# Optimization experiments

Measured on AMD Instinct MI355X. Metric: run time of the kernel, lower is better.

## Reference

```python
import jax, jax.numpy as jnp
import numpy as np

B, S, DM, H, DF = 2, 2048, 1024, 16, 4096
HD = DM // H
EPS = 1e-6
NEG = -1e9


def setup_inputs() -> dict:
    key = jax.random.key(0)
    ks = jax.random.split(key, 16)
    sc = 1.0 / np.sqrt(DM)
    scf = 1.0 / np.sqrt(DF)
    return {
        "x": jax.random.normal(ks[0], (B, S, DM), jnp.float32),
        "src_mask": jax.random.randint(ks[1], (B, 1, 1, S), 0, 2, jnp.int32),
        "Wq": jax.random.normal(ks[2], (DM, DM), jnp.float32) * sc,
        "bq": jnp.zeros((DM,), jnp.float32),
        "Wk": jax.random.normal(ks[3], (DM, DM), jnp.float32) * sc,
        "bk": jnp.zeros((DM,), jnp.float32),
        "Wv": jax.random.normal(ks[4], (DM, DM), jnp.float32) * sc,
        "bv": jnp.zeros((DM,), jnp.float32),
        "Wo": jax.random.normal(ks[5], (DM, DM), jnp.float32) * sc,
        "bo": jnp.zeros((DM,), jnp.float32),
        "W1": jax.random.normal(ks[6], (DM, DF), jnp.float32) * sc,
        "b1": jnp.zeros((DF,), jnp.float32),
        "W2": jax.random.normal(ks[7], (DF, DM), jnp.float32) * scf,
        "b2": jnp.zeros((DM,), jnp.float32),
        "alpha1": jnp.ones((1,), jnp.float32),
        "beta1": jnp.ones((1,), jnp.float32),
        "alpha2": jnp.ones((1,), jnp.float32),
        "beta2": jnp.ones((1,), jnp.float32),
    }


def layer_norm(x, alpha, beta):
    # torch: mean + unbiased std (ddof=1), scalar alpha/beta, eps added to std
    mean = jnp.mean(x, axis=-1, keepdims=True)
    std = jnp.std(x, axis=-1, keepdims=True, ddof=1)
    return alpha * (x - mean) / (std + EPS) + beta


def mha(x, mask, Wq, bq, Wk, bk, Wv, bv, Wo, bo):
    def split(t):  # [B,S,DM] -> [B,H,S,HD]
        return t.reshape(B, S, H, HD).transpose(0, 2, 1, 3)
    q = split(x @ Wq + bq)
    k = split(x @ Wk + bk)
    v = split(x @ Wv + bv)
    scores = jnp.einsum("bhqd,bhkd->bhqk", q, k) / np.sqrt(HD)
    scores = jnp.where(mask == 0, NEG, scores)
    probs = jax.nn.softmax(scores, axis=-1)  # dropout in eval mode = identity
    out = jnp.einsum("bhqk,bhkd->bhqd", probs, v)
    out = out.transpose(0, 2, 1, 3).reshape(B, S, DM)
    return out @ Wo + bo


def reference(x, src_mask, Wq, bq, Wk, bk, Wv, bv, Wo, bo, W1, b1, W2, b2,
              alpha1, beta1, alpha2, beta2):
    # pre-norm residual: x + attn(norm(x)); dropout disabled (eval)
    n1 = layer_norm(x, alpha1, beta1)
    h = x + mha(n1, src_mask, Wq, bq, Wk, bk, Wv, bv, Wo, bo)
    n2 = layer_norm(h, alpha2, beta2)
    ff = jax.nn.relu(n2 @ W1 + b1) @ W2 + b2
    return h + ff
```

## Files before the change

### kernel.cpp

```cpp
#include <hip/hip_runtime.h>
#include <hip/hip_bf16.h>

#define SEQ   2048
#define BATCH 2
#define DMODEL 1024
#define DFF   4096
#define NHEAD 16
#define HDIM  64
#define NTOK  (BATCH*SEQ)

typedef short s8v __attribute__((ext_vector_type(8)));
typedef float f4v __attribute__((ext_vector_type(4)));

__device__ __forceinline__ float b2f(unsigned short u) {
    union { unsigned int i; float f; } v; v.i = ((unsigned int)u) << 16; return v.f;
}
__device__ __forceinline__ unsigned short f2b(float f) {
    union { unsigned int i; float f; } v; v.f = f;
    unsigned int r = v.i + 0x7FFFu + ((v.i >> 16) & 1u);
    return (unsigned short)(r >> 16);
}
__device__ __forceinline__ ushort2 cvt_pk(float a, float b) {
    __hip_bfloat162 h = __float22bfloat162_rn(float2{ a, b });
    return *(ushort2*)&h;
}

__device__ __forceinline__ f4v mfma_bf16(s8v a, s8v b, f4v c) {
    return __builtin_amdgcn_mfma_f32_16x16x32_bf16(a, b, c, 0, 0, 0);
}

__device__ __forceinline__ void gload_lds16(const void* g, void* l) {
    __builtin_amdgcn_global_load_lds(
        (const __attribute__((address_space(1))) unsigned int*)g,
        (__attribute__((address_space(3))) unsigned int*)l, 16, 0, 0);
}

template<int N> __device__ __forceinline__ void wait_vmcnt() {
    if constexpr (N == 8)      asm volatile("s_waitcnt vmcnt(8)" ::: "memory");
    else if constexpr (N == 6) asm volatile("s_waitcnt vmcnt(6)" ::: "memory");
    else                       asm volatile("s_waitcnt vmcnt(0)" ::: "memory");
}

__device__ __forceinline__ void tp_tile(const float* __restrict__ src,
                                        unsigned short* __restrict__ dst,
                                        int R, int C, int br, int bc, int t,
                                        unsigned short* tl) {
    for (int i = 0; i < 16; i++) {
        int idx = t + 256 * i;
        int r = idx >> 6, c = idx & 63;
        tl[r * 65 + c] = f2b(src[(size_t)(br * 64 + r) * C + bc * 64 + c]);
    }
    __syncthreads();
    for (int i = 0; i < 16; i++) {
        int idx = t + 256 * i;
        int r2 = idx >> 6, c2 = idx & 63;
        dst[(size_t)(bc * 64 + r2) * R + br * 64 + c2] = tl[c2 * 65 + r2];
    }
}

__global__ __launch_bounds__(256) void prep_weights(const float* __restrict__ Wq,
                                                    const float* __restrict__ Wk,
                                                    const float* __restrict__ Wv,
                                                    const float* __restrict__ Wo,
                                                    const float* __restrict__ W1,
                                                    const float* __restrict__ W2,
                                                    const float* __restrict__ bq,
                                                    const float* __restrict__ bk,
                                                    const float* __restrict__ bv,
                                                    const int* __restrict__ msk,
                                                    const float* __restrict__ x,
                                                    const float* __restrict__ a1,
                                                    const float* __restrict__ be1,
                                                    unsigned short* __restrict__ Wqkv_t,
                                                    unsigned short* __restrict__ Wo_t,
                                                    unsigned short* __restrict__ W1_t,
                                                    unsigned short* __restrict__ W2_t,
                                                    float* __restrict__ bqkv,
                                                    float* __restrict__ maskf,
                                                    unsigned short* __restrict__ n1) {
    __shared__ unsigned short tl[64 * 65];
    __shared__ float red[8];
    const int t = threadIdx.x;
    const int bx = blockIdx.x, by = blockIdx.y, z = blockIdx.z;
    if (z < 4) {
        const float* src = (z == 0) ? Wq : (z == 1) ? Wk : (z == 2) ? Wv : Wo;
        unsigned short* dst = (z == 3) ? Wo_t : Wqkv_t + (size_t)z * 1024 * 1024;
        tp_tile(src, dst, 1024, 1024, bx, by, t, tl);
    } else if (z == 4) {
        for (int i = 0; i < 4; i++) {
            tp_tile(W1, W1_t, 1024, 4096, bx, by + 16 * i, t, tl);
            __syncthreads();
        }
    } else if (z == 5) {
        if (bx == 0 && by == 0) {
            for (int i = 0; i < 12; i++) {
                int idx = t + 256 * i;
                if (idx < 1024) bqkv[idx] = bq[idx];
                else if (idx < 2048) bqkv[idx] = bk[idx - 1024];
                else if (idx < 3072) bqkv[idx] = bv[idx - 2048];
            }
        }
        if (bx == 1 && by == 0) {
            for (int i = 0; i < 16; i++) {
                int idx = t + 256 * i;
                maskf[idx] = (msk[idx] == 0) ? -1e9f : 0.f;
            }
        }
        for (int i = 0; i < 4; i++) {
            tp_tile(W2, W2_t, 4096, 1024, bx + 16 * i, by, t, tl);
            __syncthreads();
        }
    } else {
        const int row = (z - 6) * 256 + by * 16 + bx;
        const float* xr = x + (size_t)row * DMODEL;
        float4 u = ((const float4*)xr)[t];
        float v[4] = { u.x, u.y, u.z, u.w };
        float s = v[0] + v[1] + v[2] + v[3];
        float sq = v[0]*v[0] + v[1]*v[1] + v[2]*v[2] + v[3]*v[3];
        for (int off = 32; off; off >>= 1) { s += __shfl_xor(s, off); sq += __shfl_xor(sq, off); }
        int wave = t >> 6, lane = t & 63;
        if (!lane) { red[wave] = s; red[4 + wave] = sq; }
        __syncthreads();
        s = red[0] + red[1] + red[2] + red[3];
        sq = red[4] + red[5] + red[6] + red[7];
        float mean = s * (1.f / DMODEL);
        float var = (sq - (float)DMODEL * mean * mean) * (1.f / (DMODEL - 1));
        var = var < 0.f ? 0.f : var;
        float inv = a1[0] / (sqrtf(var) + 1e-6f);
        float bt = be1[0];
        uint2 ou;
        unsigned short r0 = f2b((v[0] - mean) * inv + bt);
        unsigned short r1 = f2b((v[1] - mean) * inv + bt);
        unsigned short r2 = f2b((v[2] - mean) * inv + bt);
        unsigned short r3 = f2b((v[3] - mean) * inv + bt);
        ou.x = (unsigned int)r0 | ((unsigned int)r1 << 16);
        ou.y = (unsigned int)r2 | ((unsigned int)r3 << 16);
        ((uint2*)(n1 + (size_t)row * DMODEL))[t] = ou;
    }
}

__global__ __launch_bounds__(256) void pack_kv(const unsigned short* __restrict__ Kb,
                                               const unsigned short* __restrict__ Vb,
                                               unsigned short* __restrict__ Kc,
                                               unsigned short* __restrict__ Vc) {
    __shared__ unsigned short tl[64 * 65];
    const int t = threadIdx.x;
    const int kt = blockIdx.x, h = blockIdx.y, b = blockIdx.z;
    const unsigned short* srcK = Kb + (size_t)b * SEQ * 1024 + h * HDIM;
    unsigned short* dstK = Kc + ((size_t)((b * NHEAD + h) * 32 + kt)) * 4096;
    for (int i = 0; i < 2; i++) {
        int ci = t + 256 * i;
        int r = ci >> 3, cp = ci & 7;
        int cl = cp ^ (r & 7);
        *(uint4*)&dstK[ci * 8] = *(const uint4*)&srcK[(size_t)(kt * 64 + r) * 1024 + cl * 8];
    }
    const unsigned short* srcV = Vb + (size_t)b * SEQ * 1024 + h * HDIM;
    for (int i = 0; i < 16; i++) {
        int idx = t + 256 * i;
        int r = idx >> 6, c = idx & 63;
        tl[r * 65 + c] = srcV[(size_t)(kt * 64 + r) * 1024 + c];
    }
    __syncthreads();
    unsigned short* dstV = Vc + ((size_t)((b * NHEAD + h) * 32 + kt)) * 4096;
    for (int i = 0; i < 2; i++) {
        int ci = t + 256 * i;
        int r = ci >> 3, cp = ci & 7;
        int cl = cp ^ (r & 7);
        ushort4 e0, e1;
        e0.x = tl[(cl * 8 + 0) * 65 + r]; e0.y = tl[(cl * 8 + 1) * 65 + r];
        e0.z = tl[(cl * 8 + 2) * 65 + r]; e0.w = tl[(cl * 8 + 3) * 65 + r];
        e1.x = tl[(cl * 8 + 4) * 65 + r]; e1.y = tl[(cl * 8 + 5) * 65 + r];
        e1.z = tl[(cl * 8 + 6) * 65 + r]; e1.w = tl[(cl * 8 + 7) * 65 + r];
        *(ushort4*)&dstV[ci * 8]     = e0;
        *(ushort4*)&dstV[ci * 8 + 4] = e1;
    }
}

__global__ __launch_bounds__(256) void ln_kernel(const float* __restrict__ x,
                                                 const float* __restrict__ al,
                                                 const float* __restrict__ be,
                                                 unsigned short* __restrict__ o) {
    const int row = blockIdx.x;
    const float* xr = x + (size_t)row * DMODEL;
    float4 u = ((const float4*)xr)[threadIdx.x];
    float v[4] = { u.x, u.y, u.z, u.w };
    float s = v[0] + v[1] + v[2] + v[3];
    float sq = v[0]*v[0] + v[1]*v[1] + v[2]*v[2] + v[3]*v[3];
    for (int off = 32; off; off >>= 1) { s += __shfl_xor(s, off); sq += __shfl_xor(sq, off); }
    __shared__ float red[8];
    int wave = threadIdx.x >> 6, lane = threadIdx.x & 63;
    if (!lane) { red[wave] = s; red[4 + wave] = sq; }
    __syncthreads();
    s = red[0] + red[1] + red[2] + red[3];
    sq = red[4] + red[5] + red[6] + red[7];
    float mean = s * (1.f / DMODEL);
    float var = (sq - (float)DMODEL * mean * mean) * (1.f / (DMODEL - 1));
    var = var < 0.f ? 0.f : var;
    float inv = al[0] / (sqrtf(var) + 1e-6f);
    float bt = be[0];
    uint2 ou;
    unsigned short r0 = f2b((v[0] - mean) * inv + bt);
    unsigned short r1 = f2b((v[1] - mean) * inv + bt);
    unsigned short r2 = f2b((v[2] - mean) * inv + bt);
    unsigned short r3 = f2b((v[3] - mean) * inv + bt);
    ou.x = (unsigned int)r0 | ((unsigned int)r1 << 16);
    ou.y = (unsigned int)r2 | ((unsigned int)r3 << 16);
    ((uint2*)(o + (size_t)row * DMODEL))[threadIdx.x] = ou;
}

template<bool RELU, bool RES, typename CT, bool SPLIT3 = false>
__global__ __launch_bounds__(256) void gemm_bt(const unsigned short* __restrict__ A,
                                               const unsigned short* __restrict__ Bt,
                                               const float* __restrict__ bias,
                                               const float* __restrict__ res,
                                               CT* __restrict__ C,
                                               int M, int N, int K) {
    __shared__ __align__(16) unsigned short smA[128 * 32];
    __shared__ __align__(16) unsigned short smB[128 * 32];
    const int t = threadIdx.x;
    const int wave = t >> 6, lane = t & 63;
    const int quad = lane >> 4, l16 = lane & 15;
    const int wm = wave & 1, wn = wave >> 1;
    const int m0 = blockIdx.x * 128, n0 = blockIdx.y * 128;

    f4v acc[4][4] = {};

    const int c0 = t, c1 = t + 256;
    const int rA0 = c0 >> 2, sA0 = c0 & 3;
    const int rA1 = c1 >> 2, sA1 = c1 & 3;

    for (int k0 = 0; k0 < K; k0 += 32) {
        __syncthreads();
        gload_lds16(A  + (size_t)(m0 + rA0) * K + k0 + sA0 * 8, smA + c0 * 8);
        gload_lds16(A  + (size_t)(m0 + rA1) * K + k0 + sA1 * 8, smA + c1 * 8);
        gload_lds16(Bt + (size_t)(n0 + rA0) * K + k0 + sA0 * 8, smB + c0 * 8);
        gload_lds16(Bt + (size_t)(n0 + rA1) * K + k0 + sA1 * 8, smB + c1 * 8);
        __syncthreads();
        s8v a[4], b[4];
        for (int i = 0; i < 4; i++)
            a[i] = *(const s8v*)&smA[(wm * 64 + i * 16 + l16) * 32 + quad * 8];
        for (int i = 0; i < 4; i++)
            b[i] = *(const s8v*)&smB[(wn * 64 + i * 16 + l16) * 32 + quad * 8];
        for (int mi = 0; mi < 4; mi++)
            for (int ni = 0; ni < 4; ni++)
                acc[mi][ni] = mfma_bf16(a[mi], b[ni], acc[mi][ni]);
    }

    for (int mi = 0; mi < 4; mi++) {
        for (int ni = 0; ni < 4; ni++) {
            int col = n0 + wn * 64 + ni * 16 + l16;
            float bv = bias[col];
            for (int r = 0; r < 4; r++) {
                int row = m0 + wm * 64 + mi * 16 + quad * 4 + r;
                float v = acc[mi][ni][r] + bv;
                if (RELU) v = v > 0.f ? v : 0.f;
                if (RES) v += res[(size_t)row * N + col];
                size_t cidx;
                if constexpr (SPLIT3)
                    cidx = (size_t)(col >> 10) * ((size_t)NTOK * 1024)
                         + (size_t)row * 1024 + (col & 1023);
                else
                    cidx = (size_t)row * N + col;
                if constexpr (sizeof(CT) == 2)
                    C[cidx] = f2b(v);
                else
                    C[cidx] = v;
            }
        }
    }
}


template<int BROWS>
__device__ __forceinline__ void stage256(const unsigned short* __restrict__ A,
                                         const unsigned short* __restrict__ Bt,
                                         int m0, int n0, int K, int k0,
                                         unsigned short* sA, unsigned short* sB, int t) {
#pragma unroll
    for (int i = 0; i < 4; i++) {
        int ci = i * 512 + t;
        int r = ci >> 3, c = (ci & 7) ^ (r & 7);
        gload_lds16(A + (size_t)(m0 + r) * K + k0 + c * 8, sA + (size_t)ci * 8);
    }
#pragma unroll
    for (int i = 0; i < BROWS / 64; i++) {
        int ci = i * 512 + t;
        int r = ci >> 3, c = (ci & 7) ^ (r & 7);
        gload_lds16(Bt + (size_t)(n0 + r) * K + k0 + c * 8, sB + (size_t)ci * 8);
    }
}

template<int NFC>
__device__ __forceinline__ void comp256(const unsigned short* sA, const unsigned short* sB,
                                        int wm, int wn, int l16, int quad,
                                        f4v acc[8][NFC]) {
#pragma unroll
    for (int s = 0; s < 2; s++) {
        s8v b[NFC];
#pragma unroll
        for (int ni = 0; ni < NFC; ni++) {
            int r = wn * (NFC * 16) + ni * 16 + l16;
            int p = (s * 4 + quad) ^ (r & 7);
            b[ni] = *(const s8v*)&sB[r * 64 + p * 8];
        }
#pragma unroll
        for (int mi = 0; mi < 8; mi++) {
            int r = wm * 128 + mi * 16 + l16;
            int p = (s * 4 + quad) ^ (r & 7);
            s8v a = *(const s8v*)&sA[r * 64 + p * 8];
#pragma unroll
            for (int ni = 0; ni < NFC; ni++)
                acc[mi][ni] = mfma_bf16(a, b[ni], acc[mi][ni]);
        }
    }
}

template<bool RELU, bool RES, typename CT, bool SPLIT3, int BN>
__global__ __launch_bounds__(512, 2) void gemm256(const unsigned short* __restrict__ A,
                                                  const unsigned short* __restrict__ Bt,
                                                  const float* __restrict__ bias,
                                                  const float* __restrict__ res,
                                                  CT* __restrict__ C,
                                                  float* __restrict__ pbuf,
                                                  int M, int N, int K, int KS) {
    constexpr int NFC = BN / 64;
    constexpr int LPT = 4 + BN / 64;
    __shared__ __align__(16) unsigned short smA[2][256 * 64];
    __shared__ __align__(16) unsigned short smB[2][BN * 64];
    const int t = threadIdx.x;
    const int wave = t >> 6, lane = t & 63;
    const int quad = lane >> 4, l16 = lane & 15;
    const int wm = wave >> 2, wn = wave & 3;
    const int m0 = blockIdx.x * 256, n0 = blockIdx.y * BN;
    const int z = blockIdx.z;
    const int kbeg = z * KS;
    const int nt = KS >> 6;

    f4v acc[8][NFC] = {};

    stage256<BN>(A, Bt, m0, n0, K, kbeg,      smA[0], smB[0], t);
    stage256<BN>(A, Bt, m0, n0, K, kbeg + 64, smA[1], smB[1], t);
    wait_vmcnt<LPT>();
    __builtin_amdgcn_s_barrier();

    for (int it = 0; it < nt - 2; ++it) {
        const int cb = it & 1;
        __builtin_amdgcn_s_setprio(1);
        comp256<NFC>(smA[cb], smB[cb], wm, wn, l16, quad, acc);
        __builtin_amdgcn_s_setprio(0);
        asm volatile("s_waitcnt lgkmcnt(0)" ::: "memory");
        __builtin_amdgcn_s_barrier();
        stage256<BN>(A, Bt, m0, n0, K, kbeg + (it + 2) * 64, smA[cb], smB[cb], t);
        wait_vmcnt<LPT>();
        __builtin_amdgcn_s_barrier();
    }
    {
        const int cb = (nt - 2) & 1;
        __builtin_amdgcn_s_setprio(1);
        comp256<NFC>(smA[cb], smB[cb], wm, wn, l16, quad, acc);
        __builtin_amdgcn_s_setprio(0);
        asm volatile("s_waitcnt vmcnt(0)" ::: "memory");
        __builtin_amdgcn_s_barrier();
    }
    {
        const int cb = (nt - 1) & 1;
        __builtin_amdgcn_s_setprio(1);
        comp256<NFC>(smA[cb], smB[cb], wm, wn, l16, quad, acc);
        __builtin_amdgcn_s_setprio(0);
    }

#pragma unroll
    for (int mi = 0; mi < 8; mi++) {
#pragma unroll
        for (int ni = 0; ni < NFC; ni++) {
            const int col = n0 + wn * (NFC * 16) + ni * 16 + l16;
            const int row0 = m0 + wm * 128 + mi * 16 + quad * 4;
            if (z == 0) {
                const float bv = bias[col];
#pragma unroll
                for (int r = 0; r < 4; r++) {
                    float v = acc[mi][ni][r] + bv;
                    if (RELU) v = v > 0.f ? v : 0.f;
                    if (RES) v += res[(size_t)(row0 + r) * N + col];
                    size_t cidx;
                    if constexpr (SPLIT3)
                        cidx = (size_t)(col >> 10) * ((size_t)NTOK * 1024)
                             + (size_t)(row0 + r) * 1024 + (col & 1023);
                    else
                        cidx = (size_t)(row0 + r) * N + col;
                    if constexpr (sizeof(CT) == 2)
                        C[cidx] = f2b(v);
                    else
                        C[cidx] = v;
                }
            } else {
#pragma unroll
                for (int r = 0; r < 4; r++)
                    pbuf[(size_t)(z - 1) * M * N + (size_t)(row0 + r) * N + col]
                        = acc[mi][ni][r];
            }
        }
    }
}

__global__ __launch_bounds__(256) void add_pbuf(float* __restrict__ out,
                                                const float* __restrict__ pbuf) {
    const int i0 = (blockIdx.x * 256 + threadIdx.x) * 8;
    float4 a0 = *(const float4*)&out[i0];
    float4 a1 = *(const float4*)&out[i0 + 4];
    float4 p0 = *(const float4*)&pbuf[i0];
    float4 p1 = *(const float4*)&pbuf[i0 + 4];
    a0.x += p0.x; a0.y += p0.y; a0.z += p0.z; a0.w += p0.w;
    a1.x += p1.x; a1.y += p1.y; a1.z += p1.z; a1.w += p1.w;
    *(float4*)&out[i0]     = a0;
    *(float4*)&out[i0 + 4] = a1;
}

__global__ __launch_bounds__(256) void attn_kernel(const unsigned short* __restrict__ Qb,
                                                   const unsigned short* __restrict__ Kc,
                                                   const unsigned short* __restrict__ Vc,
                                                   const float* __restrict__ maskf,
                                                   unsigned short* __restrict__ out) {
    __shared__ __align__(16) unsigned short smK[4096];
    __shared__ __align__(16) unsigned short smV[4096];
    __shared__ __align__(16) unsigned short smP[4][16 * 72];

    const int t = threadIdx.x;
    const int wave = t >> 6, lane = t & 63;
    const int quad = lane >> 4, l16 = lane & 15;
    const int qt = blockIdx.x, h = blockIdx.y, b = blockIdx.z;
    const int q0 = qt * 64 + wave * 16;
    const unsigned short* Kbh = Kc + ((size_t)(b * NHEAD + h)) * 32 * 4096;
    const unsigned short* Vbh = Vc + ((size_t)(b * NHEAD + h)) * 32 * 4096;
    const float* mrow = maskf + b * SEQ;
    unsigned short* smPw = &smP[wave][0];

    const unsigned short* Qp = Qb + ((size_t)b * SEQ + q0 + l16) * 1024 + h * HDIM + quad * 8;
    s8v qf0 = *(const s8v*)(Qp);
    s8v qf1 = *(const s8v*)(Qp + 32);

    float l_s = 0.f;
    f4v oacc[4] = {};

    for (int kt = 0; kt < 32; kt++) {
        const int k0 = kt * 64;
        const unsigned short* ks = Kbh + kt * 4096;
        const unsigned short* vs = Vbh + kt * 4096;
        __syncthreads();
        gload_lds16(ks + t * 8,           smK + t * 8);
        gload_lds16(ks + (t + 256) * 8,   smK + (t + 256) * 8);
        gload_lds16(vs + t * 8,           smV + t * 8);
        gload_lds16(vs + (t + 256) * 8,   smV + (t + 256) * 8);
        __syncthreads();

        f4v s[4];
        for (int kt4 = 0; kt4 < 4; kt4++) {
            int r = kt4 * 16 + l16, sw = r & 7;
            s8v kf0 = *(const s8v*)&smK[r * 64 + ((quad ^ sw) * 8)];
            s8v kf1 = *(const s8v*)&smK[r * 64 + (((quad + 4) ^ sw) * 8)];
            f4v z = {};
            z = mfma_bf16(kf0, qf0, z);
            z = mfma_bf16(kf1, qf1, z);
            s[kt4] = z;
        }
        for (int kt4 = 0; kt4 < 4; kt4++) {
            float4 mf = *(const float4*)&mrow[k0 + kt4 * 16 + quad * 4];
            s[kt4][0] = s[kt4][0] * 0.125f + mf.x;
            s[kt4][1] = s[kt4][1] * 0.125f + mf.y;
            s[kt4][2] = s[kt4][2] * 0.125f + mf.z;
            s[kt4][3] = s[kt4][3] * 0.125f + mf.w;
        }
        for (int kt4 = 0; kt4 < 4; kt4++)
            for (int r = 0; r < 4; r++) {
                float p = __expf(s[kt4][r]);
                s[kt4][r] = p;
                l_s += p;
            }
        for (int kt4 = 0; kt4 < 4; kt4++) {
            ushort2 p01 = cvt_pk(s[kt4][0], s[kt4][1]);
            ushort2 p23 = cvt_pk(s[kt4][2], s[kt4][3]);
            ushort4 pk;
            pk.x = p01.x; pk.y = p01.y; pk.z = p23.x; pk.w = p23.y;
            *(ushort4*)&smPw[l16 * 72 + kt4 * 16 + quad * 4] = pk;
        }
        s8v pf0 = *(const s8v*)&smPw[l16 * 72 + quad * 8];
        s8v pf1 = *(const s8v*)&smPw[l16 * 72 + quad * 8 + 32];
        for (int nt = 0; nt < 4; nt++) {
            int r = nt * 16 + l16, sw = r & 7;
            s8v v0 = *(const s8v*)&smV[r * 64 + ((quad ^ sw) * 8)];
            s8v v1 = *(const s8v*)&smV[r * 64 + (((quad + 4) ^ sw) * 8)];
            oacc[nt] = mfma_bf16(pf0, v0, oacc[nt]);
            oacc[nt] = mfma_bf16(pf1, v1, oacc[nt]);
        }
    }

    l_s += __shfl_xor(l_s, 16);
    l_s += __shfl_xor(l_s, 32);
    float lrr[4];
    for (int r = 0; r < 4; r++) lrr[r] = __shfl(l_s, quad * 4 + r);
    for (int nt = 0; nt < 4; nt++)
        for (int r = 0; r < 4; r++) {
            int row = q0 + quad * 4 + r;
            int col = h * HDIM + nt * 16 + l16;
            out[((size_t)b * SEQ + row) * DMODEL + col] = f2b(oacc[nt][r] / lrr[r]);
        }
}

extern "C" void kernel_launch(void* const* d_in, const int* in_sizes, int n_in,
                              void* d_out, int out_size, void* d_ws, size_t ws_size,
                              hipStream_t stream) {
    const float* x   = (const float*)d_in[0];
    const int*   msk = (const int*)d_in[1];
    const float* Wq  = (const float*)d_in[2];
    const float* bq  = (const float*)d_in[3];
    const float* Wk  = (const float*)d_in[4];
    const float* bk  = (const float*)d_in[5];
    const float* Wv  = (const float*)d_in[6];
    const float* bv  = (const float*)d_in[7];
    const float* Wo  = (const float*)d_in[8];
    const float* bo  = (const float*)d_in[9];
    const float* W1  = (const float*)d_in[10];
    const float* b1  = (const float*)d_in[11];
    const float* W2  = (const float*)d_in[12];
    const float* b2  = (const float*)d_in[13];
    const float* a1  = (const float*)d_in[14];
    const float* be1 = (const float*)d_in[15];
    const float* a2  = (const float*)d_in[16];
    const float* be2 = (const float*)d_in[17];
    float* outf = (float*)d_out;

    char* ws = (char*)d_ws;
    const size_t MB = 1024 * 1024;
    unsigned short* W2_t   = (unsigned short*)(ws);
    unsigned short* W1_t   = (unsigned short*)(ws + 8 * MB);
    float*          Pbuf   = (float*)(ws + 8 * MB);
    unsigned short* Wqkv_t = (unsigned short*)(ws + 16 * MB);
    float*          bqkv   = (float*)(ws + 22 * MB);
    unsigned short* Kc     = (unsigned short*)(ws + 16 * MB);
    unsigned short* n2     = (unsigned short*)(ws + 16 * MB);
    unsigned short* Wo_t   = (unsigned short*)(ws + 24 * MB);
    unsigned short* Qb     = (unsigned short*)(ws + 26 * MB);
    unsigned short* Kb     = (unsigned short*)(ws + 34 * MB);
    unsigned short* Vb     = (unsigned short*)(ws + 42 * MB);
    unsigned short* ff1    = (unsigned short*)(ws + 26 * MB);
    unsigned short* attnO  = (unsigned short*)(ws + 50 * MB);
    unsigned short* n1     = (unsigned short*)d_out;
    float*          maskf  = (float*)((char*)d_out + 8 * MB);
    unsigned short* Vc     = (unsigned short*)d_out;
    float*          hbuf   = (float*)d_out;

    prep_weights<<<dim3(16, 16, 22), 256, 0, stream>>>(
        Wq, Wk, Wv, Wo, W1, W2, bq, bk, bv, msk, x, a1, be1,
        Wqkv_t, Wo_t, W1_t, W2_t, bqkv, maskf, n1);

    gemm256<false, false, unsigned short, true, 256><<<dim3(16, 12, 1), 512, 0, stream>>>(
        n1, Wqkv_t, bqkv, nullptr, Qb, nullptr, NTOK, 3072, 1024, 1024);
    pack_kv<<<dim3(32, 16, 2), 256, 0, stream>>>(Kb, Vb, Kc, Vc);
    attn_kernel<<<dim3(32, 16, 2), 256, 0, stream>>>(Qb, Kc, Vc, maskf, attnO);
    gemm_bt<false, true, float><<<dim3(32, 8), 256, 0, stream>>>(
        attnO, Wo_t, bo, x, hbuf, NTOK, 1024, 1024);
    ln_kernel<<<NTOK, 256, 0, stream>>>(hbuf, a2, be2, n2);
    gemm256<true, false, unsigned short, false, 256><<<dim3(16, 16, 1), 512, 0, stream>>>(
        n2, W1_t, b1, nullptr, ff1, nullptr, NTOK, DFF, 1024, 1024);
    gemm256<false, true, float, false, 128><<<dim3(16, 8, 2), 512, 0, stream>>>(
        ff1, W2_t, b2, hbuf, outf, Pbuf, NTOK, 1024, 4096, 2048);
    add_pbuf<<<dim3(2048), 256, 0, stream>>>(outf, Pbuf);
}
```

Baseline: 381.0 us.

## Double-buffer attention K/V tiles and move Wo projection to split-K gemm256

The attention kernel now runs 512 threads per block (128 queries) and double-buffers K/V tiles in LDS. It prefetches the next tile with async global-to-LDS loads while the current one is computed, stages the mask in LDS, and uses a swizzled P buffer with raised wave priority. The output projection drops the old 128x128 gemm_bt for the larger-tile gemm256 path with split-K over two partial buffers plus an add_pbuf pass. The intent is to hide load latency and reuse K/V across more queries, at the cost of an extra launch and more LDS per block.

```diff
diff --git a/kernel.cpp b/kernel.cpp
--- a/kernel.cpp
+++ b/kernel.cpp
@@ -38,6 +38,7 @@
 template<int N> __device__ __forceinline__ void wait_vmcnt() {
     if constexpr (N == 8)      asm volatile("s_waitcnt vmcnt(8)" ::: "memory");
     else if constexpr (N == 6) asm volatile("s_waitcnt vmcnt(6)" ::: "memory");
+    else if constexpr (N == 2) asm volatile("s_waitcnt vmcnt(2)" ::: "memory");
     else                       asm volatile("s_waitcnt vmcnt(0)" ::: "memory");
 }
 
@@ -208,69 +209,6 @@
     ((uint2*)(o + (size_t)row * DMODEL))[threadIdx.x] = ou;
 }
 
-template<bool RELU, bool RES, typename CT, bool SPLIT3 = false>
-__global__ __launch_bounds__(256) void gemm_bt(const unsigned short* __restrict__ A,
-                                               const unsigned short* __restrict__ Bt,
-                                               const float* __restrict__ bias,
-                                               const float* __restrict__ res,
-                                               CT* __restrict__ C,
-                                               int M, int N, int K) {
-    __shared__ __align__(16) unsigned short smA[128 * 32];
-    __shared__ __align__(16) unsigned short smB[128 * 32];
-    const int t = threadIdx.x;
-    const int wave = t >> 6, lane = t & 63;
-    const int quad = lane >> 4, l16 = lane & 15;
-    const int wm = wave & 1, wn = wave >> 1;
-    const int m0 = blockIdx.x * 128, n0 = blockIdx.y * 128;
-
-    f4v acc[4][4] = {};
-
-    const int c0 = t, c1 = t + 256;
-    const int rA0 = c0 >> 2, sA0 = c0 & 3;
-    const int rA1 = c1 >> 2, sA1 = c1 & 3;
-
-    for (int k0 = 0; k0 < K; k0 += 32) {
-        __syncthreads();
-        gload_lds16(A  + (size_t)(m0 + rA0) * K + k0 + sA0 * 8, smA + c0 * 8);
-        gload_lds16(A  + (size_t)(m0 + rA1) * K + k0 + sA1 * 8, smA + c1 * 8);
-        gload_lds16(Bt + (size_t)(n0 + rA0) * K + k0 + sA0 * 8, smB + c0 * 8);
-        gload_lds16(Bt + (size_t)(n0 + rA1) * K + k0 + sA1 * 8, smB + c1 * 8);
-        __syncthreads();
-        s8v a[4], b[4];
-        for (int i = 0; i < 4; i++)
-            a[i] = *(const s8v*)&smA[(wm * 64 + i * 16 + l16) * 32 + quad * 8];
-        for (int i = 0; i < 4; i++)
-            b[i] = *(const s8v*)&smB[(wn * 64 + i * 16 + l16) * 32 + quad * 8];
-        for (int mi = 0; mi < 4; mi++)
-            for (int ni = 0; ni < 4; ni++)
-                acc[mi][ni] = mfma_bf16(a[mi], b[ni], acc[mi][ni]);
-    }
-
-    for (int mi = 0; mi < 4; mi++) {
-        for (int ni = 0; ni < 4; ni++) {
-            int col = n0 + wn * 64 + ni * 16 + l16;
-            float bv = bias[col];
-            for (int r = 0; r < 4; r++) {
-                int row = m0 + wm * 64 + mi * 16 + quad * 4 + r;
-                float v = acc[mi][ni][r] + bv;
-                if (RELU) v = v > 0.f ? v : 0.f;
-                if (RES) v += res[(size_t)row * N + col];
-                size_t cidx;
-                if constexpr (SPLIT3)
-                    cidx = (size_t)(col >> 10) * ((size_t)NTOK * 1024)
-                         + (size_t)row * 1024 + (col & 1023);
-                else
-                    cidx = (size_t)row * N + col;
-                if constexpr (sizeof(CT) == 2)
-                    C[cidx] = f2b(v);
-                else
-                    C[cidx] = v;
-            }
-        }
-    }
-}
-
-
 template<int BROWS>
 __device__ __forceinline__ void stage256(const unsigned short* __restrict__ A,
                                          const unsigned short* __restrict__ Bt,
@@ -416,82 +354,118 @@
     *(float4*)&out[i0 + 4] = a1;
 }
 
-__global__ __launch_bounds__(256) void attn_kernel(const unsigned short* __restrict__ Qb,
+__device__ __forceinline__ void attn_tile(const unsigned short* __restrict__ smKb,
+                                          const unsigned short* __restrict__ smVb,
+                                          const float* __restrict__ smM, int k0,
+                                          unsigned short* __restrict__ smPw,
+                                          s8v qf0, s8v qf1, int quad, int l16,
+                                          float& l_s, f4v* oacc) {
+    const int l7 = l16 & 7;
+    f4v s[4];
+#pragma unroll
+    for (int kt4 = 0; kt4 < 4; kt4++) {
+        int r = kt4 * 16 + l16;
+        s8v kf0 = *(const s8v*)&smKb[r * 64 + ((quad ^ l7) * 8)];
+        s8v kf1 = *(const s8v*)&smKb[r * 64 + (((quad + 4) ^ l7) * 8)];
+        f4v z = {};
+        z = mfma_bf16(kf0, qf0, z);
+        z = mfma_bf16(kf1, qf1, z);
+        s[kt4] = z;
+    }
+#pragma unroll
+    for (int kt4 = 0; kt4 < 4; kt4++) {
+        float4 mf = *(const float4*)&smM[k0 + kt4 * 16 + quad * 4];
+        s[kt4][0] = s[kt4][0] * 0.125f + mf.x;
+        s[kt4][1] = s[kt4][1] * 0.125f + mf.y;
+        s[kt4][2] = s[kt4][2] * 0.125f + mf.z;
+        s[kt4][3] = s[kt4][3] * 0.125f + mf.w;
+    }
+#pragma unroll
+    for (int kt4 = 0; kt4 < 4; kt4++)
+#pragma unroll
+        for (int r = 0; r < 4; r++) {
+            float p = __expf(s[kt4][r]);
+            s[kt4][r] = p;
+            l_s += p;
+        }
+#pragma unroll
+    for (int kt4 = 0; kt4 < 4; kt4++) {
+        ushort2 p01 = cvt_pk(s[kt4][0], s[kt4][1]);
+        ushort2 p23 = cvt_pk(s[kt4][2], s[kt4][3]);
+        ushort4 pk;
+        pk.x = p01.x; pk.y = p01.y; pk.z = p23.x; pk.w = p23.y;
+        int c = kt4 * 2 + (quad >> 1);
+        *(ushort4*)&smPw[l16 * 64 + ((c ^ l7) * 8 + (quad & 1) * 4)] = pk;
+    }
+    s8v pf0 = *(const s8v*)&smPw[l16 * 64 + ((quad ^ l7) * 8)];
+    s8v pf1 = *(const s8v*)&smPw[l16 * 64 + (((quad + 4) ^ l7) * 8)];
+#pragma unroll
+    for (int nt = 0; nt < 4; nt++) {
+        int r = nt * 16 + l16;
+        s8v v0 = *(const s8v*)&smVb[r * 64 + ((quad ^ l7) * 8)];
+        s8v v1 = *(const s8v*)&smVb[r * 64 + (((quad + 4) ^ l7) * 8)];
+        oacc[nt] = mfma_bf16(pf0, v0, oacc[nt]);
+        oacc[nt] = mfma_bf16(pf1, v1, oacc[nt]);
+    }
+}
+
+__global__ __launch_bounds__(512) void attn_kernel(const unsigned short* __restrict__ Qb,
                                                    const unsigned short* __restrict__ Kc,
                                                    const unsigned short* __restrict__ Vc,
                                                    const float* __restrict__ maskf,
                                                    unsigned short* __restrict__ out) {
-    __shared__ __align__(16) unsigned short smK[4096];
-    __shared__ __align__(16) unsigned short smV[4096];
-    __shared__ __align__(16) unsigned short smP[4][16 * 72];
+    __shared__ __align__(16) unsigned short smK[2][4096];
+    __shared__ __align__(16) unsigned short smV[2][4096];
+    __shared__ __align__(16) unsigned short smP[8][1024];
+    __shared__ __align__(16) float smM[SEQ];
 
     const int t = threadIdx.x;
     const int wave = t >> 6, lane = t & 63;
     const int quad = lane >> 4, l16 = lane & 15;
     const int qt = blockIdx.x, h = blockIdx.y, b = blockIdx.z;
-    const int q0 = qt * 64 + wave * 16;
+    const int q0 = qt * 128 + wave * 16;
     const unsigned short* Kbh = Kc + ((size_t)(b * NHEAD + h)) * 32 * 4096;
     const unsigned short* Vbh = Vc + ((size_t)(b * NHEAD + h)) * 32 * 4096;
-    const float* mrow = maskf + b * SEQ;
     unsigned short* smPw = &smP[wave][0];
 
     const unsigned short* Qp = Qb + ((size_t)b * SEQ + q0 + l16) * 1024 + h * HDIM + quad * 8;
     s8v qf0 = *(const s8v*)(Qp);
     s8v qf1 = *(const s8v*)(Qp + 32);
 
+    gload_lds16(maskf + (size_t)b * SEQ + t * 4, (float*)smM + t * 4);
+    gload_lds16(Kbh + t * 8,        smK[0] + t * 8);
+    gload_lds16(Vbh + t * 8,        smV[0] + t * 8);
+    gload_lds16(Kbh + 4096 + t * 8, smK[1] + t * 8);
+    gload_lds16(Vbh + 4096 + t * 8, smV[1] + t * 8);
+    wait_vmcnt<2>();
+    __builtin_amdgcn_s_barrier();
+
     float l_s = 0.f;
     f4v oacc[4] = {};
 
-    for (int kt = 0; kt < 32; kt++) {
-        const int k0 = kt * 64;
-        const unsigned short* ks = Kbh + kt * 4096;
-        const unsigned short* vs = Vbh + kt * 4096;
-        __syncthreads();
-        gload_lds16(ks + t * 8,           smK + t * 8);
-        gload_lds16(ks + (t + 256) * 8,   smK + (t + 256) * 8);
-        gload_lds16(vs + t * 8,           smV + t * 8);
-        gload_lds16(vs + (t + 256) * 8,   smV + (t + 256) * 8);
-        __syncthreads();
-
-        f4v s[4];
-        for (int kt4 = 0; kt4 < 4; kt4++) {
-            int r = kt4 * 16 + l16, sw = r & 7;
-            s8v kf0 = *(const s8v*)&smK[r * 64 + ((quad ^ sw) * 8)];
-            s8v kf1 = *(const s8v*)&smK[r * 64 + (((quad + 4) ^ sw) * 8)];
-            f4v z = {};
-            z = mfma_bf16(kf0, qf0, z);
-            z = mfma_bf16(kf1, qf1, z);
-            s[kt4] = z;
-        }
-        for (int kt4 = 0; kt4 < 4; kt4++) {
-            float4 mf = *(const float4*)&mrow[k0 + kt4 * 16 + quad * 4];
-            s[kt4][0] = s[kt4][0] * 0.125f + mf.x;
-            s[kt4][1] = s[kt4][1] * 0.125f + mf.y;
-            s[kt4][2] = s[kt4][2] * 0.125f + mf.z;
-            s[kt4][3] = s[kt4][3] * 0.125f + mf.w;
-        }
-        for (int kt4 = 0; kt4 < 4; kt4++)
-            for (int r = 0; r < 4; r++) {
-                float p = __expf(s[kt4][r]);
-                s[kt4][r] = p;
-                l_s += p;
-            }
-        for (int kt4 = 0; kt4 < 4; kt4++) {
-            ushort2 p01 = cvt_pk(s[kt4][0], s[kt4][1]);
-            ushort2 p23 = cvt_pk(s[kt4][2], s[kt4][3]);
-            ushort4 pk;
-            pk.x = p01.x; pk.y = p01.y; pk.z = p23.x; pk.w = p23.y;
-            *(ushort4*)&smPw[l16 * 72 + kt4 * 16 + quad * 4] = pk;
-        }
-        s8v pf0 = *(const s8v*)&smPw[l16 * 72 + quad * 8];
-        s8v pf1 = *(const s8v*)&smPw[l16 * 72 + quad * 8 + 32];
-        for (int nt = 0; nt < 4; nt++) {
-            int r = nt * 16 + l16, sw = r & 7;
-            s8v v0 = *(const s8v*)&smV[r * 64 + ((quad ^ sw) * 8)];
-            s8v v1 = *(const s8v*)&smV[r * 64 + (((quad + 4) ^ sw) * 8)];
-            oacc[nt] = mfma_bf16(pf0, v0, oacc[nt]);
-            oacc[nt] = mfma_bf16(pf1, v1, oacc[nt]);
-        }
+    for (int it = 0; it < 30; ++it) {
+        const int cb = it & 1;
+        __builtin_amdgcn_s_setprio(1);
+        attn_tile(smK[cb], smV[cb], smM, it * 64, smPw, qf0, qf1, quad, l16, l_s, oacc);
+        __builtin_amdgcn_s_setprio(0);
+        asm volatile("s_waitcnt lgkmcnt(0)" ::: "memory");
+        __builtin_amdgcn_s_barrier();
+        gload_lds16(Kbh + (size_t)(it + 2) * 4096 + t * 8, smK[cb] + t * 8);
+        gload_lds16(Vbh + (size_t)(it + 2) * 4096 + t * 8, smV[cb] + t * 8);
+        wait_vmcnt<2>();
+        __builtin_amdgcn_s_barrier();
+    }
+    {
+        __builtin_amdgcn_s_setprio(1);
+        attn_tile(smK[0], smV[0], smM, 30 * 64, smPw, qf0, qf1, quad, l16, l_s, oacc);
+        __builtin_amdgcn_s_setprio(0);
+        wait_vmcnt<0>();
+        __builtin_amdgcn_s_barrier();
+    }
+    {
+        __builtin_amdgcn_s_setprio(1);
+        attn_tile(smK[1], smV[1], smM, 31 * 64, smPw, qf0, qf1, quad, l16, l_s, oacc);
+        __builtin_amdgcn_s_setprio(0);
     }
 
     l_s += __shfl_xor(l_s, 16);
@@ -542,6 +516,7 @@
     unsigned short* Qb     = (unsigned short*)(ws + 26 * MB);
     unsigned short* Kb     = (unsigned short*)(ws + 34 * MB);
     unsigned short* Vb     = (unsigned short*)(ws + 42 * MB);
+    float*          Pbuf2  = (float*)(ws + 34 * MB);
     unsigned short* ff1    = (unsigned short*)(ws + 26 * MB);
     unsigned short* attnO  = (unsigned short*)(ws + 50 * MB);
     unsigned short* n1     = (unsigned short*)d_out;
@@ -556,9 +531,10 @@
     gemm256<false, false, unsigned short, true, 256><<<dim3(16, 12, 1), 512, 0, stream>>>(
         n1, Wqkv_t, bqkv, nullptr, Qb, nullptr, NTOK, 3072, 1024, 1024);
     pack_kv<<<dim3(32, 16, 2), 256, 0, stream>>>(Kb, Vb, Kc, Vc);
-    attn_kernel<<<dim3(32, 16, 2), 256, 0, stream>>>(Qb, Kc, Vc, maskf, attnO);
-    gemm_bt<false, true, float><<<dim3(32, 8), 256, 0, stream>>>(
-        attnO, Wo_t, bo, x, hbuf, NTOK, 1024, 1024);
+    attn_kernel<<<dim3(16, 16, 2), 512, 0, stream>>>(Qb, Kc, Vc, maskf, attnO);
+    gemm256<false, true, float, false, 128><<<dim3(16, 8, 2), 512, 0, stream>>>(
+        attnO, Wo_t, bo, x, hbuf, Pbuf2, NTOK, 1024, 1024, 512);
+    add_pbuf<<<dim3(2048), 256, 0, stream>>>(hbuf, Pbuf2);
     ln_kernel<<<NTOK, 256, 0, stream>>>(hbuf, a2, be2, n2);
     gemm256<true, false, unsigned short, false, 256><<<dim3(16, 16, 1), 512, 0, stream>>>(
         n2, W1_t, b1, nullptr, ff1, nullptr, NTOK, DFF, 1024, 1024);
```

Result: faster. 372.4 us (-2.2%).
